# Performance work log

Measured on AMD Instinct MI355X. Metric: run time of the kernel, lower is better.

## Reference

```python
import jax, jax.numpy as jnp
import numpy as np

OBS_DIM, ACTION_DIM, H, FC = 64, 100, 512, 256
IN_DIM = FC + ACTION_DIM


def setup_inputs() -> dict:
    key = jax.random.key(0)
    ks = jax.random.split(key, 10)
    s = lambda k, shp, fan: jax.random.normal(k, shp, jnp.float32) * (1.0 / np.sqrt(fan))
    return {
        "observations": jax.random.normal(ks[0], (32, 2048, OBS_DIM), jnp.float32),
        "actions": jax.random.uniform(ks[1], (32, 2048), jnp.float32),
        "W_obs": s(ks[2], (OBS_DIM, FC), OBS_DIM), "b_obs": jnp.zeros((FC,), jnp.float32),
        "W_act": s(ks[3], (1, ACTION_DIM), 1), "b_act": jnp.zeros((ACTION_DIM,), jnp.float32),
        "W_lstm": s(ks[4], (IN_DIM, 4 * H), IN_DIM),
        "U_lstm": s(ks[5], (H, 4 * H), H),
        "b_lstm": jnp.zeros((4 * H,), jnp.float32),
        "W_proj": s(ks[6], (H, ACTION_DIM), H), "b_proj": jnp.zeros((ACTION_DIM,), jnp.float32),
    }


def _lstm_seq(x, W, U, b):
    # x: [B, T, D] -> outputs [B, T, H]; keras LSTMCell default activations.
    B = x.shape[0]
    h0 = jnp.zeros((B, H), x.dtype)
    c0 = jnp.zeros((B, H), x.dtype)

    def step(carry, x_t):
        h, c = carry
        z = x_t @ W + h @ U + b  # [B, 4H]
        i, f, g, o = jnp.split(z, 4, axis=-1)
        i = jax.nn.sigmoid(i); f = jax.nn.sigmoid(f)
        g = jnp.tanh(g); o = jax.nn.sigmoid(o)
        c = f * c + i * g
        h = o * jnp.tanh(c)
        return (h, c), h

    _, hs = jax.lax.scan(step, (h0, c0), jnp.swapaxes(x, 0, 1))  # [T, B, H]
    return jnp.swapaxes(hs, 0, 1)


def reference(observations, actions, W_obs, b_obs, W_act, b_act,
              W_lstm, U_lstm, b_lstm, W_proj, b_proj):
    a = jax.nn.relu(actions[..., None] @ W_act + b_act)        # [B, T, A]
    ob = jax.nn.relu(observations @ W_obs + b_obs)             # [B, T, FC]
    x = jnp.concatenate([ob, a], axis=-1)                      # [B, T, FC+A]
    seq = _lstm_seq(x, W_lstm, U_lstm, b_lstm)                 # [B, T, H]
    logits = seq @ W_proj + b_proj                             # [B, T, A]
    pi = jax.nn.softmax(logits, axis=-1)
    # tf.math.argmax(logits) defaults to axis=0 (over batch), kept faithfully.
    argmax_actions = jnp.argmax(logits, axis=0)
    return pi, logits, argmax_actions
```

## Files before the change

### kernel.cpp

```cpp
#include <hip/hip_runtime.h>
#include <cstdint>
#include <cstddef>

#define B_   32
#define T_   2048
#define OBS_ 64
#define FC_  256
#define ACT_ 100
#define H_   512
#define TC_  128
#define NCH_ 16

typedef __attribute__((ext_vector_type(4))) unsigned int u32x4;
typedef __attribute__((ext_vector_type(8))) short bf16x8;
typedef __attribute__((ext_vector_type(4))) float f32x4;

static __device__ __forceinline__ bf16x8 as_b(u32x4 v){ union{u32x4 u; bf16x8 b;} x; x.u=v; return x.b; }
static __device__ __forceinline__ unsigned short f2bf(float f){
  unsigned int u = __builtin_bit_cast(unsigned int, f);
  return (unsigned short)((u + 0x7fffu + ((u>>16)&1u)) >> 16);
}
static __device__ __forceinline__ float bf2f(unsigned short s){
  unsigned int u = ((unsigned int)s) << 16;
  return __builtin_bit_cast(float, u);
}
static __device__ __forceinline__ void split3(float v, unsigned short& h, unsigned short& m, unsigned short& l){
  h = f2bf(v);
  float r1 = v - bf2f(h);
  m = f2bf(r1);
  float r2 = r1 - bf2f(m);
  l = f2bf(r2);
}
static __device__ __forceinline__ u32x4 pack8(const unsigned short* v){
  u32x4 r;
  r.x = (unsigned)v[0] | ((unsigned)v[1]<<16);
  r.y = (unsigned)v[2] | ((unsigned)v[3]<<16);
  r.z = (unsigned)v[4] | ((unsigned)v[5]<<16);
  r.w = (unsigned)v[6] | ((unsigned)v[7]<<16);
  return r;
}
static __device__ __forceinline__ u32x4 load_cohx4(const unsigned int* p){
  u32x4 r;
  asm volatile("global_load_dwordx4 %0, %1, off sc0 sc1"
               : "=v"(r) : "v"(p) : "memory");
  return r;
}

static constexpr size_t XF_OFF    = 0;
static constexpr size_t XF_SZ     = (size_t)TC_*2*12*3*64*16;
static constexpr size_t WF_OFF    = XF_OFF + XF_SZ;
static constexpr size_t WF_SZ     = (size_t)32*4*28*3*64*16;
static constexpr size_t WPF_OFF   = WF_OFF + WF_SZ;
static constexpr size_t WPF_SZ    = (size_t)7*16*3*64*16;
static constexpr size_t ZX_OFF    = WPF_OFF + WPF_SZ;
static constexpr size_t ZX_SZ     = (size_t)TC_*2*16*2048*4;
static constexpr size_t HC01_OFF  = ZX_OFF + ZX_SZ;
static constexpr size_t HC01_SZ   = (size_t)TC_*2*16*512*4;
static constexpr size_t HC2_OFF   = HC01_OFF + HC01_SZ;
static constexpr size_t HC2_SZ    = (size_t)TC_*2*16*512*2;
static constexpr size_t HG_OFF    = HC2_OFF + HC2_SZ;
static constexpr size_t HG_SZ     = (size_t)3*2*16*2*256*4;
static constexpr size_t CST_OFF   = HG_OFF + HG_SZ;
static constexpr size_t CST_SZ    = (size_t)B_*H_*8;
static constexpr size_t CTR_OFF   = CST_OFF + CST_SZ;
static constexpr size_t CTR_SZ    = (size_t)2*T_*4;

__global__ __launch_bounds__(256) void k_prep_x(
    const float* __restrict__ obs, const float* __restrict__ act,
    const float* __restrict__ Wobs, const float* __restrict__ bobs,
    const float* __restrict__ Wact, const float* __restrict__ bact,
    u32x4* __restrict__ Xf, int tbase)
{
  __shared__ float Wl[64][257];
  __shared__ float ol[32][64];
  __shared__ float xr[32][256];
  __shared__ float al[32];
  __shared__ float wal[100], bal[100], bol[256];
  int tl = blockIdx.x; int t = tbase + tl; int tid = threadIdx.x;
  for (int i = tid; i < 64*256; i += 256) Wl[i>>8][i&255] = Wobs[i];
  for (int i = tid; i < 32*64; i += 256)
    ol[i>>6][i&63] = obs[((size_t)(i>>6)*T_ + t)*OBS_ + (i&63)];
  if (tid < 32) al[tid] = act[(size_t)tid*T_ + t];
  if (tid < 100) { wal[tid] = Wact[tid]; bal[tid] = bact[tid]; }
  bol[tid] = bobs[tid];
  __syncthreads();
  {
    int k = tid;
    double accd[32];
#pragma unroll
    for (int r = 0; r < 32; ++r) accd[r] = 0.0;
    for (int kc = 0; kc < 64; kc += 8) {
      float w[8];
#pragma unroll
      for (int q = 0; q < 8; ++q) w[q] = Wl[kc+q][k];
#pragma unroll
      for (int r = 0; r < 32; ++r) {
#pragma unroll
        for (int q = 0; q < 8; ++q) accd[r] += (double)w[q]*(double)ol[r][kc+q];
      }
    }
#pragma unroll
    for (int r = 0; r < 32; ++r) xr[r][k] = fmaxf((float)(accd[r] + (double)bol[k]), 0.f);
  }
  __syncthreads();
  int g = tid >> 6, l = tid & 63;
  int r = l & 15, sub = l >> 4;
  for (int p = g; p < 24; p += 4) {
    int bg = p / 12, kk = p % 12;
    int b = bg*16 + r;
    unsigned short vh[8], vm[8], vl[8];
#pragma unroll
    for (int j = 0; j < 8; ++j) {
      int k = kk*32 + sub*8 + j;
      float x;
      if (k < 256)      x = xr[b][k];
      else if (k < 356) {
        double tmp = (double)al[b]*(double)wal[k-256] + (double)bal[k-256];
        x = fmaxf((float)tmp, 0.f);
      } else            x = 0.f;
      split3(x, vh[j], vm[j], vl[j]);
    }
    size_t base = ((((size_t)tl*2 + bg)*12 + kk)*3)*64 + l;
    Xf[base]       = pack8(vh);
    Xf[base + 64]  = pack8(vm);
    Xf[base + 128] = pack8(vl);
  }
}

__global__ __launch_bounds__(256) void k_prep_w(
    const float* __restrict__ Wl, const float* __restrict__ Ul,
    unsigned short* __restrict__ Wf)
{
  size_t gid = (size_t)blockIdx.x*256 + threadIdx.x;
  if (gid >= (size_t)896*2048) return;
  int k = (int)(gid >> 11), oc = (int)(gid & 2047);
  float v = 0.f;
  if (k < 356) v = Wl[(size_t)k*2048 + oc];
  else if (k >= 384) v = Ul[(size_t)(k-384)*2048 + oc];
  unsigned short vh, vm, vlo;
  split3(v, vh, vm, vlo);
  int g = oc >> 9, hs = (oc & 511) >> 4, u = oc & 15;
  int kk = k >> 5, sub = (k >> 3) & 3, j = k & 7;
  size_t e = ((((size_t)(hs*4 + g)*28 + kk)*3 + 0)*64 + (sub*16 + u))*8 + j;
  Wf[e]        = vh;
  Wf[e + 512]  = vm;
  Wf[e + 1024] = vlo;
}

__global__ __launch_bounds__(256) void k_prep_wp(
    const float* __restrict__ Wp, unsigned short* __restrict__ Wpf)
{
  int gid = blockIdx.x*256 + threadIdx.x;
  if (gid >= 512*112) return;
  int k = gid / 112, c = gid % 112;
  float v = (c < 100) ? Wp[(size_t)k*100 + c] : 0.f;
  unsigned short vh, vm, vlo;
  split3(v, vh, vm, vlo);
  int ct = c >> 4, cl = c & 15;
  int kk = k >> 5, sub = (k >> 3) & 3, j = k & 7;
  size_t e = (((size_t)(ct*16 + kk)*3 + 0)*64 + (sub*16 + cl))*8 + j;
  Wpf[e]        = vh;
  Wpf[e + 512]  = vm;
  Wpf[e + 1024] = vlo;
}

__global__ __launch_bounds__(256) void k_prep_zx(
    const u32x4* __restrict__ Xf, const u32x4* __restrict__ Wf,
    float* __restrict__ zx)
{
  int bid = blockIdx.x;
  int hq = bid & 7, bg = (bid >> 3) & 1, tl = bid >> 4;
  int tid = threadIdx.x;
  int g = tid >> 6, lane = tid & 63;
  u32x4 xa[12][3];
  const u32x4* xp = Xf + (((size_t)tl*2 + bg)*12*3)*64 + lane;
#pragma unroll
  for (int f = 0; f < 12; ++f)
#pragma unroll
    for (int p = 0; p < 3; ++p) xa[f][p] = xp[(f*3+p)*64];
  for (int hi = 0; hi < 4; ++hi) {
    int hs = hq*4 + hi;
    const u32x4* bp = Wf + (((size_t)(hs*4 + g)*28)*3)*64 + lane;
    f32x4 a0={0,0,0,0},a1={0,0,0,0},a2={0,0,0,0},a3={0,0,0,0},a4={0,0,0,0},a5={0,0,0,0};
#pragma unroll
    for (int f = 0; f < 12; ++f) {
      u32x4 b0 = bp[(f*3+0)*64], b1 = bp[(f*3+1)*64], b2 = bp[(f*3+2)*64];
      a0 = __builtin_amdgcn_mfma_f32_16x16x32_bf16(as_b(xa[f][0]), as_b(b0), a0, 0,0,0);
      a1 = __builtin_amdgcn_mfma_f32_16x16x32_bf16(as_b(xa[f][0]), as_b(b1), a1, 0,0,0);
      a2 = __builtin_amdgcn_mfma_f32_16x16x32_bf16(as_b(xa[f][1]), as_b(b0), a2, 0,0,0);
      a3 = __builtin_amdgcn_mfma_f32_16x16x32_bf16(as_b(xa[f][0]), as_b(b2), a3, 0,0,0);
      a4 = __builtin_amdgcn_mfma_f32_16x16x32_bf16(as_b(xa[f][2]), as_b(b0), a4, 0,0,0);
      a5 = __builtin_amdgcn_mfma_f32_16x16x32_bf16(as_b(xa[f][1]), as_b(b1), a5, 0,0,0);
    }
    int col = lane & 15;
#pragma unroll
    for (int q = 0; q < 4; ++q) {
      int row = (lane>>4)*4 + q;
      double z = (((double)a3[q]+(double)a4[q])+(double)a5[q])
               + ((double)a1[q]+(double)a2[q]) + (double)a0[q];
      zx[(((size_t)tl*2 + bg)*16 + row)*2048 + g*512 + hs*16 + col] = (float)z;
    }
  }
}

__global__ __launch_bounds__(256, 1) void k_rnn(
    const u32x4* __restrict__ Wf, const float* __restrict__ zx,
    const float* __restrict__ blstm,
    unsigned int* __restrict__ HC01, unsigned short* __restrict__ HC2,
    unsigned int* __restrict__ hg32, int* __restrict__ ctr,
    double* __restrict__ cstate, int tbase)
{
  __shared__ double zbuf[4][16][16];
  __shared__ unsigned int hb01[16][16];
  int wg = blockIdx.x, bg = wg >> 5, hs = wg & 31;
  int tid = threadIdx.x, w = tid >> 6, lane = tid & 63;
  u32x4 Breg[16][3];
  {
    const u32x4* bp = Wf + (((size_t)(hs*4 + w)*28 + 12)*3)*64 + lane;
#pragma unroll
    for (int f = 0; f < 16; ++f)
#pragma unroll
      for (int p = 0; p < 3; ++p) Breg[f][p] = bp[(f*3+p)*64];
  }
  int gr = tid >> 4, gu = tid & 15;
  double bi  = (double)blstm[0*512 + hs*16 + gu];
  double bff = (double)blstm[1*512 + hs*16 + gu];
  double bgg = (double)blstm[2*512 + hs*16 + gu];
  double bo  = (double)blstm[3*512 + hs*16 + gu];
  double c = cstate[(size_t)(bg*16 + gr)*512 + hs*16 + gu];
  int r2 = tid >> 3, p8 = tid & 7;
  int hg0 = hs*16 + 2*p8;
  int pkk = hg0 >> 5, psub = (hg0 >> 3) & 3, pj = hg0 & 7;
  int plw = psub*16 + r2;

#pragma unroll 1
  for (int tl = 0; tl < TC_; ++tl) {
    int gt = tbase + tl;
    int sr = (gt + 2) % 3;
    u32x4 hf[16][2];
    {
      const unsigned int* hbase = hg32 + ((size_t)sr*2 + bg)*16*2*256 + lane*4;
#pragma unroll
      for (int kk = 0; kk < 16; ++kk) {
        hf[kk][0] = load_cohx4(hbase + ((size_t)kk*2 + 0)*256);
        hf[kk][1] = load_cohx4(hbase + ((size_t)kk*2 + 1)*256);
      }
    }
    size_t zrow = (((size_t)tl*2 + bg)*16 + gr)*2048 + hs*16 + gu;
    float z0 = zx[zrow];
    float z1 = zx[zrow + 512];
    float z2 = zx[zrow + 1024];
    float z3 = zx[zrow + 1536];
    asm volatile("s_waitcnt vmcnt(0)" ::: "memory");
    __builtin_amdgcn_sched_barrier(0);
    f32x4 a0={0,0,0,0},a1={0,0,0,0},a2={0,0,0,0},a3={0,0,0,0},a4={0,0,0,0};
#pragma unroll
    for (int kk = 0; kk < 16; ++kk) {
      a0 = __builtin_amdgcn_mfma_f32_16x16x32_bf16(as_b(hf[kk][0]), as_b(Breg[kk][0]), a0, 0,0,0);
      a1 = __builtin_amdgcn_mfma_f32_16x16x32_bf16(as_b(hf[kk][0]), as_b(Breg[kk][1]), a1, 0,0,0);
      a2 = __builtin_amdgcn_mfma_f32_16x16x32_bf16(as_b(hf[kk][1]), as_b(Breg[kk][0]), a2, 0,0,0);
      a3 = __builtin_amdgcn_mfma_f32_16x16x32_bf16(as_b(hf[kk][0]), as_b(Breg[kk][2]), a3, 0,0,0);
      a4 = __builtin_amdgcn_mfma_f32_16x16x32_bf16(as_b(hf[kk][1]), as_b(Breg[kk][1]), a4, 0,0,0);
    }
#pragma unroll
    for (int q = 0; q < 4; ++q)
      zbuf[w][(lane>>4)*4 + q][lane & 15] =
        (((double)a3[q] + (double)a4[q]) + ((double)a1[q] + (double)a2[q])) + (double)a0[q];
    __syncthreads();
    {
      double zi = zbuf[0][gr][gu] + (double)z0 + bi;
      double zf = zbuf[1][gr][gu] + (double)z1 + bff;
      double zg = zbuf[2][gr][gu] + (double)z2 + bgg;
      double zo = zbuf[3][gr][gu] + (double)z3 + bo;
      double i_ = 1.0/(1.0 + exp(-zi));
      double f_ = 1.0/(1.0 + exp(-zf));
      double g_ = tanh(zg);
      double o_ = 1.0/(1.0 + exp(-zo));
      c = f_*c + i_*g_;
      double h = o_*tanh(c);
      unsigned short h0, h1, h2;
      split3((float)h, h0, h1, h2);
      unsigned int w01 = (unsigned)h0 | ((unsigned)h1 << 16);
      size_t hcidx = (((size_t)tl*2 + bg)*16 + gr)*512 + hs*16 + gu;
      HC01[hcidx] = w01;
      HC2[hcidx]  = h2;
      hb01[gr][gu] = w01;
    }
    __syncthreads();
    if (tid < 128) {
      unsigned int a = hb01[r2][2*p8], b = hb01[r2][2*p8+1];
      unsigned int v0 = (a & 0xffffu) | (b << 16);
      unsigned int v1 = (a >> 16)     | (b & 0xffff0000u);
      size_t dg = ((((size_t)(gt%3)*2 + bg)*16 + pkk)*2 + 0)*256 + plw*4 + (pj>>1);
      __hip_atomic_store(&hg32[dg],       v0, __ATOMIC_RELAXED, __HIP_MEMORY_SCOPE_AGENT);
      __hip_atomic_store(&hg32[dg + 256], v1, __ATOMIC_RELAXED, __HIP_MEMORY_SCOPE_AGENT);
    }
    __syncthreads();
    if (tid == 0) {
      __hip_atomic_fetch_add(&ctr[bg*T_ + gt], 1, __ATOMIC_RELAXED, __HIP_MEMORY_SCOPE_AGENT);
      while (__hip_atomic_load(&ctr[bg*T_ + gt], __ATOMIC_RELAXED, __HIP_MEMORY_SCOPE_AGENT) < 32)
        __builtin_amdgcn_s_sleep(1);
    }
    __syncthreads();
  }
  cstate[(size_t)(bg*16 + gr)*512 + hs*16 + gu] = c;
}

__global__ __launch_bounds__(256) void k_logits(
    const unsigned int* __restrict__ HC01, const unsigned short* __restrict__ HC2,
    const u32x4* __restrict__ Wpf,
    const float* __restrict__ bproj, float* __restrict__ out, int tbase)
{
  __shared__ float zl[16][120];
  int bid = blockIdx.x;
  int tl = bid >> 1, bg = bid & 1;
  int tid = threadIdx.x;
  int w = tid >> 6, lane = tid & 63;
  int row = lane & 15, koff = (lane >> 4) * 8;
  u32x4 a[16][3];
  {
    const unsigned int* h01 = HC01 + (((size_t)tl*2 + bg)*16 + row)*512 + koff;
    const unsigned short* h2p = HC2 + (((size_t)tl*2 + bg)*16 + row)*512 + koff;
#pragma unroll
    for (int kk = 0; kk < 16; ++kk) {
      u32x4 c0 = *(const u32x4*)(h01 + 32*kk);
      u32x4 c1 = *(const u32x4*)(h01 + 32*kk + 4);
      u32x4 p0, p1;
      p0.x = (c0.x & 0xffffu) | (c0.y << 16);
      p0.y = (c0.z & 0xffffu) | (c0.w << 16);
      p0.z = (c1.x & 0xffffu) | (c1.y << 16);
      p0.w = (c1.z & 0xffffu) | (c1.w << 16);
      p1.x = (c0.x >> 16) | (c0.y & 0xffff0000u);
      p1.y = (c0.z >> 16) | (c0.w & 0xffff0000u);
      p1.z = (c1.x >> 16) | (c1.y & 0xffff0000u);
      p1.w = (c1.z >> 16) | (c1.w & 0xffff0000u);
      a[kk][0] = p0;
      a[kk][1] = p1;
      a[kk][2] = *(const u32x4*)(h2p + 32*kk);
    }
  }
  for (int ct = w; ct < 7; ct += 4) {
    f32x4 c0 = {0,0,0,0}, c1 = {0,0,0,0}, c2 = {0,0,0,0};
    f32x4 c3 = {0,0,0,0}, c4 = {0,0,0,0}, c5 = {0,0,0,0};
    const u32x4* bp2 = Wpf + ((size_t)ct*16*3)*64 + lane;
#pragma unroll
    for (int kk = 0; kk < 16; ++kk) {
      u32x4 b0 = bp2[(kk*3+0)*64], b1 = bp2[(kk*3+1)*64], b2 = bp2[(kk*3+2)*64];
      c0 = __builtin_amdgcn_mfma_f32_16x16x32_bf16(as_b(a[kk][0]), as_b(b0), c0, 0,0,0);
      c1 = __builtin_amdgcn_mfma_f32_16x16x32_bf16(as_b(a[kk][0]), as_b(b1), c1, 0,0,0);
      c2 = __builtin_amdgcn_mfma_f32_16x16x32_bf16(as_b(a[kk][1]), as_b(b0), c2, 0,0,0);
      c3 = __builtin_amdgcn_mfma_f32_16x16x32_bf16(as_b(a[kk][0]), as_b(b2), c3, 0,0,0);
      c4 = __builtin_amdgcn_mfma_f32_16x16x32_bf16(as_b(a[kk][2]), as_b(b0), c4, 0,0,0);
      c5 = __builtin_amdgcn_mfma_f32_16x16x32_bf16(as_b(a[kk][1]), as_b(b1), c5, 0,0,0);
    }
    int col = ct*16 + (lane & 15);
    float bv = (col < 100) ? bproj[col] : 0.f;
#pragma unroll
    for (int q = 0; q < 4; ++q) {
      double z = (((double)c3[q] + (double)c4[q]) + (double)c5[q])
               + ((double)c1[q] + (double)c2[q]) + (double)c0[q] + (double)bv;
      if (col < 120) zl[(lane>>4)*4 + q][col] = (float)z;
    }
  }
  __syncthreads();
  int srow = tid >> 4, l16 = tid & 15;
  float vv[7];
  float m = -1e30f;
#pragma unroll
  for (int k2 = 0; k2 < 7; ++k2) {
    int col = l16 + 16*k2;
    vv[k2] = (col < 100) ? zl[srow][col] : -1e30f;
    m = fmaxf(m, vv[k2]);
  }
#pragma unroll
  for (int d = 1; d < 16; d <<= 1) m = fmaxf(m, __shfl_xor(m, d, 64));
  float s = 0.f; float ek[7];
#pragma unroll
  for (int k2 = 0; k2 < 7; ++k2) {
    int col = l16 + 16*k2;
    ek[k2] = (col < 100) ? expf(vv[k2] - m) : 0.f;
    s += ek[k2];
  }
#pragma unroll
  for (int d = 1; d < 16; d <<= 1) s += __shfl_xor(s, d, 64);
  int t = tbase + tl; int b = bg*16 + srow;
  float* piout = out;
  float* lgout = out + 6553600ull;
#pragma unroll
  for (int k2 = 0; k2 < 7; ++k2) {
    int col = l16 + 16*k2;
    if (col < 100) {
      size_t idx = ((size_t)b*T_ + t)*100 + col;
      lgout[idx] = vv[k2];
      piout[idx] = ek[k2] / s;
    }
  }
}

__global__ __launch_bounds__(128) void k_argmax(
    const float* __restrict__ lg, float* __restrict__ outA)
{
  int t = blockIdx.x, j = threadIdx.x;
  if (j >= 100) return;
  float best = lg[(size_t)t*100 + j];
  int bi = 0;
  for (int b = 1; b < 32; ++b) {
    float v = lg[((size_t)b*T_ + t)*100 + j];
    if (v > best) { best = v; bi = b; }
  }
  outA[(size_t)t*100 + j] = (float)bi;
}

extern "C" void kernel_launch(void* const* d_in, const int* in_sizes, int n_in,
                              void* d_out, int out_size, void* d_ws, size_t ws_size,
                              hipStream_t stream) {
  const float* obs  = (const float*)d_in[0];
  const float* act  = (const float*)d_in[1];
  const float* Wobs = (const float*)d_in[2];
  const float* bobs = (const float*)d_in[3];
  const float* Wact = (const float*)d_in[4];
  const float* bact = (const float*)d_in[5];
  const float* Wl   = (const float*)d_in[6];
  const float* Ul   = (const float*)d_in[7];
  const float* bl   = (const float*)d_in[8];
  const float* Wp   = (const float*)d_in[9];
  const float* bp   = (const float*)d_in[10];
  char* ws = (char*)d_ws;
  u32x4* Xf             = (u32x4*)(ws + XF_OFF);
  unsigned short* WfS   = (unsigned short*)(ws + WF_OFF);
  unsigned short* WpfS  = (unsigned short*)(ws + WPF_OFF);
  float* zx             = (float*)(ws + ZX_OFF);
  unsigned int* HC01    = (unsigned int*)(ws + HC01_OFF);
  unsigned short* HC2   = (unsigned short*)(ws + HC2_OFF);
  unsigned int* hg32    = (unsigned int*)(ws + HG_OFF);
  double* cstate        = (double*)(ws + CST_OFF);
  int* ctr              = (int*)(ws + CTR_OFF);
  float* out = (float*)d_out;

  hipMemsetAsync(ws + HG_OFF, 0, HG_SZ + CST_SZ + CTR_SZ, stream);
  k_prep_w<<<7168, 256, 0, stream>>>(Wl, Ul, WfS);
  k_prep_wp<<<(512*112 + 255)/256, 256, 0, stream>>>(Wp, WpfS);
  for (int ch = 0; ch < NCH_; ++ch) {
    int tb = ch * TC_;
    k_prep_x<<<TC_, 256, 0, stream>>>(obs, act, Wobs, bobs, Wact, bact, Xf, tb);
    k_prep_zx<<<TC_*2*8, 256, 0, stream>>>((const u32x4*)Xf, (const u32x4*)WfS, zx);
    k_rnn<<<64, 256, 0, stream>>>((const u32x4*)WfS, zx, bl, HC01, HC2,
                                  hg32, ctr, cstate, tb);
    k_logits<<<TC_*2, 256, 0, stream>>>(HC01, HC2, (const u32x4*)WpfS, bp, out, tb);
  }
  k_argmax<<<T_, 128, 0, stream>>>(out + 6553600ull, out + 13107200ull);
}
```

Before: 10.61 ms.

## Interleave LSTM gate columns so each lane computes gates without LDS round-trips

New measurement: 12.99 ms. 22.4% more time.

```diff
diff --git a/kernel.cpp b/kernel.cpp
--- a/kernel.cpp
+++ b/kernel.cpp
@@ -42,7 +42,7 @@
 static __device__ __forceinline__ u32x4 load_cohx4(const unsigned int* p){
   u32x4 r;
   asm volatile("global_load_dwordx4 %0, %1, off sc0 sc1"
-               : "=v"(r) : "v"(p) : "memory");
+               : "=&v"(r) : "v"(p) : "memory");
   return r;
 }
 
@@ -53,7 +53,7 @@
 static constexpr size_t WPF_OFF   = WF_OFF + WF_SZ;
 static constexpr size_t WPF_SZ    = (size_t)7*16*3*64*16;
 static constexpr size_t ZX_OFF    = WPF_OFF + WPF_SZ;
-static constexpr size_t ZX_SZ     = (size_t)TC_*2*16*2048*4;
+static constexpr size_t ZX_SZ     = (size_t)TC_*2*2048*16*4;
 static constexpr size_t HC01_OFF  = ZX_OFF + ZX_SZ;
 static constexpr size_t HC01_SZ   = (size_t)TC_*2*16*512*4;
 static constexpr size_t HC2_OFF   = HC01_OFF + HC01_SZ;
@@ -61,7 +61,7 @@
 static constexpr size_t HG_OFF    = HC2_OFF + HC2_SZ;
 static constexpr size_t HG_SZ     = (size_t)3*2*16*2*256*4;
 static constexpr size_t CST_OFF   = HG_OFF + HG_SZ;
-static constexpr size_t CST_SZ    = (size_t)B_*H_*8;
+static constexpr size_t CST_SZ    = (size_t)B_*H_*4;
 static constexpr size_t CTR_OFF   = CST_OFF + CST_SZ;
 static constexpr size_t CTR_SZ    = (size_t)2*T_*4;
 
@@ -139,9 +139,11 @@
   else if (k >= 384) v = Ul[(size_t)(k-384)*2048 + oc];
   unsigned short vh, vm, vlo;
   split3(v, vh, vm, vlo);
-  int g = oc >> 9, hs = (oc & 511) >> 4, u = oc & 15;
+  int g = oc >> 9, hu = oc & 511;
+  int hs = hu >> 4, wv = (hu >> 2) & 3, u = hu & 3;
+  int cc = g*4 + u;
   int kk = k >> 5, sub = (k >> 3) & 3, j = k & 7;
-  size_t e = ((((size_t)(hs*4 + g)*28 + kk)*3 + 0)*64 + (sub*16 + u))*8 + j;
+  size_t e = ((((size_t)(hs*4 + wv)*28 + kk)*3 + 0)*64 + (sub*16 + cc))*8 + j;
   Wf[e]        = vh;
   Wf[e + 512]  = vm;
   Wf[e + 1024] = vlo;
@@ -166,12 +168,14 @@
 
 __global__ __launch_bounds__(256) void k_prep_zx(
     const u32x4* __restrict__ Xf, const u32x4* __restrict__ Wf,
-    float* __restrict__ zx)
+    const float* __restrict__ blstm, float* __restrict__ zxT)
 {
   int bid = blockIdx.x;
   int hq = bid & 7, bg = (bid >> 3) & 1, tl = bid >> 4;
   int tid = threadIdx.x;
-  int g = tid >> 6, lane = tid & 63;
+  int v = tid >> 6, lane = tid & 63;
+  int cc = lane & 15; int g = cc >> 2, u = cc & 3;
+  int rbase = (lane >> 4) * 4;
   u32x4 xa[12][3];
   const u32x4* xp = Xf + (((size_t)tl*2 + bg)*12*3)*64 + lane;
 #pragma unroll
@@ -180,7 +184,7 @@
     for (int p = 0; p < 3; ++p) xa[f][p] = xp[(f*3+p)*64];
   for (int hi = 0; hi < 4; ++hi) {
     int hs = hq*4 + hi;
-    const u32x4* bp = Wf + (((size_t)(hs*4 + g)*28)*3)*64 + lane;
+    const u32x4* bp = Wf + (((size_t)(hs*4 + v)*28)*3)*64 + lane;
     f32x4 a0={0,0,0,0},a1={0,0,0,0},a2={0,0,0,0},a3={0,0,0,0},a4={0,0,0,0},a5={0,0,0,0};
 #pragma unroll
     for (int f = 0; f < 12; ++f) {
@@ -192,118 +196,132 @@
       a4 = __builtin_amdgcn_mfma_f32_16x16x32_bf16(as_b(xa[f][2]), as_b(b0), a4, 0,0,0);
       a5 = __builtin_amdgcn_mfma_f32_16x16x32_bf16(as_b(xa[f][1]), as_b(b1), a5, 0,0,0);
     }
-    int col = lane & 15;
+    int oc = g*512 + hs*16 + v*4 + u;
+    double bb = (double)blstm[oc];
+    f32x4 st;
 #pragma unroll
     for (int q = 0; q < 4; ++q) {
-      int row = (lane>>4)*4 + q;
       double z = (((double)a3[q]+(double)a4[q])+(double)a5[q])
-               + ((double)a1[q]+(double)a2[q]) + (double)a0[q];
-      zx[(((size_t)tl*2 + bg)*16 + row)*2048 + g*512 + hs*16 + col] = (float)z;
-    }
+               + ((double)a1[q]+(double)a2[q]) + (double)a0[q] + bb;
+      st[q] = (float)z;
+    }
+    *(f32x4*)(zxT + ((size_t)((size_t)(tl*2 + bg)*2048 + oc))*16 + rbase) = st;
   }
 }
 
 __global__ __launch_bounds__(256, 1) void k_rnn(
-    const u32x4* __restrict__ Wf, const float* __restrict__ zx,
-    const float* __restrict__ blstm,
+    const u32x4* __restrict__ Wf, const float* __restrict__ zxT,
     unsigned int* __restrict__ HC01, unsigned short* __restrict__ HC2,
     unsigned int* __restrict__ hg32, int* __restrict__ ctr,
-    double* __restrict__ cstate, int tbase)
-{
-  __shared__ double zbuf[4][16][16];
-  __shared__ unsigned int hb01[16][16];
+    float* __restrict__ cstate, int tbase)
+{
   int wg = blockIdx.x, bg = wg >> 5, hs = wg & 31;
-  int tid = threadIdx.x, w = tid >> 6, lane = tid & 63;
+  int tid = threadIdx.x, wv = tid >> 6, lane = tid & 63;
+  int cc = lane & 15;
+  int g = cc >> 2, u = cc & 3;
+  int rbase = (lane >> 4) * 4;
+  int U = hs*16 + wv*4 + u;
   u32x4 Breg[16][3];
   {
-    const u32x4* bp = Wf + (((size_t)(hs*4 + w)*28 + 12)*3)*64 + lane;
+    const u32x4* bp = Wf + ((((size_t)(hs*4 + wv)*28) + 12)*3)*64 + lane;
 #pragma unroll
     for (int f = 0; f < 16; ++f)
 #pragma unroll
       for (int p = 0; p < 3; ++p) Breg[f][p] = bp[(f*3+p)*64];
-  }
-  int gr = tid >> 4, gu = tid & 15;
-  double bi  = (double)blstm[0*512 + hs*16 + gu];
-  double bff = (double)blstm[1*512 + hs*16 + gu];
-  double bgg = (double)blstm[2*512 + hs*16 + gu];
-  double bo  = (double)blstm[3*512 + hs*16 + gu];
-  double c = cstate[(size_t)(bg*16 + gr)*512 + hs*16 + gu];
-  int r2 = tid >> 3, p8 = tid & 7;
-  int hg0 = hs*16 + 2*p8;
-  int pkk = hg0 >> 5, psub = (hg0 >> 3) & 3, pj = hg0 & 7;
-  int plw = psub*16 + r2;
+#pragma unroll
+    for (int f = 0; f < 16; ++f)
+#pragma unroll
+      for (int p = 0; p < 3; ++p) asm volatile("" : "+v"(Breg[f][p]));
+  }
+  float c[4];
+#pragma unroll
+  for (int q = 0; q < 4; ++q)
+    c[q] = cstate[(size_t)(bg*16 + rbase + q)*512 + U];
+  int Ue = hs*16 + wv*4 + (u & 2);
+  int wkk = Ue >> 5, wsub = (Ue >> 3) & 3, wwrd = (Ue >> 1) & 3;
 
 #pragma unroll 1
   for (int tl = 0; tl < TC_; ++tl) {
     int gt = tbase + tl;
-    int sr = (gt + 2) % 3;
-    u32x4 hf[16][2];
+    u32x4 hf0[16], hf1[16];
     {
-      const unsigned int* hbase = hg32 + ((size_t)sr*2 + bg)*16*2*256 + lane*4;
+      const unsigned int* hbase = hg32 + ((size_t)((gt+2)%3)*2 + bg)*16*2*256 + lane*4;
 #pragma unroll
       for (int kk = 0; kk < 16; ++kk) {
-        hf[kk][0] = load_cohx4(hbase + ((size_t)kk*2 + 0)*256);
-        hf[kk][1] = load_cohx4(hbase + ((size_t)kk*2 + 1)*256);
+        hf0[kk] = load_cohx4(hbase + (kk*2+0)*256);
+        hf1[kk] = load_cohx4(hbase + (kk*2+1)*256);
       }
     }
-    size_t zrow = (((size_t)tl*2 + bg)*16 + gr)*2048 + hs*16 + gu;
-    float z0 = zx[zrow];
-    float z1 = zx[zrow + 512];
-    float z2 = zx[zrow + 1024];
-    float z3 = zx[zrow + 1536];
+    f32x4 zx = *(const f32x4*)(zxT + ((size_t)((size_t)(tl*2 + bg)*2048 + g*512 + U))*16 + rbase);
     asm volatile("s_waitcnt vmcnt(0)" ::: "memory");
     __builtin_amdgcn_sched_barrier(0);
     f32x4 a0={0,0,0,0},a1={0,0,0,0},a2={0,0,0,0},a3={0,0,0,0},a4={0,0,0,0};
 #pragma unroll
     for (int kk = 0; kk < 16; ++kk) {
-      a0 = __builtin_amdgcn_mfma_f32_16x16x32_bf16(as_b(hf[kk][0]), as_b(Breg[kk][0]), a0, 0,0,0);
-      a1 = __builtin_amdgcn_mfma_f32_16x16x32_bf16(as_b(hf[kk][0]), as_b(Breg[kk][1]), a1, 0,0,0);
-      a2 = __builtin_amdgcn_mfma_f32_16x16x32_bf16(as_b(hf[kk][1]), as_b(Breg[kk][0]), a2, 0,0,0);
-      a3 = __builtin_amdgcn_mfma_f32_16x16x32_bf16(as_b(hf[kk][0]), as_b(Breg[kk][2]), a3, 0,0,0);
-      a4 = __builtin_amdgcn_mfma_f32_16x16x32_bf16(as_b(hf[kk][1]), as_b(Breg[kk][1]), a4, 0,0,0);
-    }
-#pragma unroll
-    for (int q = 0; q < 4; ++q)
-      zbuf[w][(lane>>4)*4 + q][lane & 15] =
-        (((double)a3[q] + (double)a4[q]) + ((double)a1[q] + (double)a2[q])) + (double)a0[q];
-    __syncthreads();
-    {
-      double zi = zbuf[0][gr][gu] + (double)z0 + bi;
-      double zf = zbuf[1][gr][gu] + (double)z1 + bff;
-      double zg = zbuf[2][gr][gu] + (double)z2 + bgg;
-      double zo = zbuf[3][gr][gu] + (double)z3 + bo;
-      double i_ = 1.0/(1.0 + exp(-zi));
-      double f_ = 1.0/(1.0 + exp(-zf));
-      double g_ = tanh(zg);
-      double o_ = 1.0/(1.0 + exp(-zo));
-      c = f_*c + i_*g_;
-      double h = o_*tanh(c);
-      unsigned short h0, h1, h2;
-      split3((float)h, h0, h1, h2);
-      unsigned int w01 = (unsigned)h0 | ((unsigned)h1 << 16);
-      size_t hcidx = (((size_t)tl*2 + bg)*16 + gr)*512 + hs*16 + gu;
-      HC01[hcidx] = w01;
-      HC2[hcidx]  = h2;
-      hb01[gr][gu] = w01;
-    }
-    __syncthreads();
-    if (tid < 128) {
-      unsigned int a = hb01[r2][2*p8], b = hb01[r2][2*p8+1];
-      unsigned int v0 = (a & 0xffffu) | (b << 16);
-      unsigned int v1 = (a >> 16)     | (b & 0xffff0000u);
-      size_t dg = ((((size_t)(gt%3)*2 + bg)*16 + pkk)*2 + 0)*256 + plw*4 + (pj>>1);
-      __hip_atomic_store(&hg32[dg],       v0, __ATOMIC_RELAXED, __HIP_MEMORY_SCOPE_AGENT);
-      __hip_atomic_store(&hg32[dg + 256], v1, __ATOMIC_RELAXED, __HIP_MEMORY_SCOPE_AGENT);
-    }
-    __syncthreads();
-    if (tid == 0) {
-      __hip_atomic_fetch_add(&ctr[bg*T_ + gt], 1, __ATOMIC_RELAXED, __HIP_MEMORY_SCOPE_AGENT);
-      while (__hip_atomic_load(&ctr[bg*T_ + gt], __ATOMIC_RELAXED, __HIP_MEMORY_SCOPE_AGENT) < 32)
-        __builtin_amdgcn_s_sleep(1);
-    }
-    __syncthreads();
-  }
-  cstate[(size_t)(bg*16 + gr)*512 + hs*16 + gu] = c;
+      a0 = __builtin_amdgcn_mfma_f32_16x16x32_bf16(as_b(hf0[kk]), as_b(Breg[kk][0]), a0, 0,0,0);
+      a1 = __builtin_amdgcn_mfma_f32_16x16x32_bf16(as_b(hf0[kk]), as_b(Breg[kk][1]), a1, 0,0,0);
+      a2 = __builtin_amdgcn_mfma_f32_16x16x32_bf16(as_b(hf1[kk]), as_b(Breg[kk][0]), a2, 0,0,0);
+      a3 = __builtin_amdgcn_mfma_f32_16x16x32_bf16(as_b(hf0[kk]), as_b(Breg[kk][2]), a3, 0,0,0);
+      a4 = __builtin_amdgcn_mfma_f32_16x16x32_bf16(as_b(hf1[kk]), as_b(Breg[kk][1]), a4, 0,0,0);
+    }
+    float hv[4];
+#pragma unroll
+    for (int q = 0; q < 4; ++q) {
+      float z = (float)(((double)a3[q] + (double)a4[q])
+                      + ((double)a1[q] + (double)a2[q]) + (double)a0[q]) + zx[q];
+      float o0 = __shfl_xor(z, 4, 64);
+      float e0 = (g & 1) ? o0 : z;
+      float e1 = (g & 1) ? z  : o0;
+      float p0 = __shfl_xor(e0, 8, 64);
+      float p1 = __shfl_xor(e1, 8, 64);
+      float zi = (g & 2) ? p0 : e0;
+      float zf = (g & 2) ? p1 : e1;
+      float zg = (g & 2) ? e0 : p0;
+      float zo = (g & 2) ? e1 : p1;
+      float i_ = 1.f/(1.f + expf(-zi));
+      float f_ = 1.f/(1.f + expf(-zf));
+      float g_ = tanhf(zg);
+      float o_ = 1.f/(1.f + expf(-zo));
+      c[q] = f_*c[q] + i_*g_;
+      hv[q] = o_*tanhf(c[q]);
+    }
+    unsigned int* ringW = hg32 + ((size_t)(gt%3)*2 + bg)*16*2*256;
+#pragma unroll
+    for (int q = 0; q < 4; ++q) {
+      float hq = hv[q];
+      float hp = __shfl_xor(hq, 1, 64);
+      unsigned short h0o = f2bf(hq);
+      float r1 = hq - bf2f(h0o);
+      unsigned short h1o = f2bf(r1);
+      if (g == 0) {
+        unsigned short h2o = f2bf(r1 - bf2f(h1o));
+        size_t hcidx = ((size_t)(tl*2 + bg)*16 + rbase + q)*512 + U;
+        HC01[hcidx] = (unsigned)h0o | ((unsigned)h1o << 16);
+        HC2[hcidx]  = h2o;
+        if (!(u & 1)) {
+          unsigned short h0p = f2bf(hp);
+          unsigned short h1p = f2bf(hp - bf2f(h0p));
+          unsigned int w0 = (unsigned)h0o | ((unsigned)h0p << 16);
+          unsigned int w1 = (unsigned)h1o | ((unsigned)h1p << 16);
+          size_t d0 = ((size_t)wkk*2 + 0)*256 + (wsub*16 + rbase + q)*4 + wwrd;
+          __hip_atomic_store(&ringW[d0],       w0, __ATOMIC_RELAXED, __HIP_MEMORY_SCOPE_AGENT);
+          __hip_atomic_store(&ringW[d0 + 256], w1, __ATOMIC_RELAXED, __HIP_MEMORY_SCOPE_AGENT);
+        }
+      }
+    }
+    if (tl < TC_-1) {
+      __syncthreads();
+      if (tid == 0) {
+        __hip_atomic_fetch_add(&ctr[bg*T_ + gt], 1, __ATOMIC_RELAXED, __HIP_MEMORY_SCOPE_AGENT);
+        while (__hip_atomic_load(&ctr[bg*T_ + gt], __ATOMIC_RELAXED, __HIP_MEMORY_SCOPE_AGENT) < 32)
+          __builtin_amdgcn_s_sleep(1);
+      }
+      __syncthreads();
+    }
+  }
+#pragma unroll
+  for (int q = 0; q < 4; ++q)
+    if (g == 0) cstate[(size_t)(bg*16 + rbase + q)*512 + U] = c[q];
 }
 
 __global__ __launch_bounds__(256) void k_logits(
@@ -429,11 +447,11 @@
   u32x4* Xf             = (u32x4*)(ws + XF_OFF);
   unsigned short* WfS   = (unsigned short*)(ws + WF_OFF);
   unsigned short* WpfS  = (unsigned short*)(ws + WPF_OFF);
-  float* zx             = (float*)(ws + ZX_OFF);
+  float* zxT            = (float*)(ws + ZX_OFF);
   unsigned int* HC01    = (unsigned int*)(ws + HC01_OFF);
   unsigned short* HC2   = (unsigned short*)(ws + HC2_OFF);
   unsigned int* hg32    = (unsigned int*)(ws + HG_OFF);
-  double* cstate        = (double*)(ws + CST_OFF);
+  float* cstate         = (float*)(ws + CST_OFF);
   int* ctr              = (int*)(ws + CTR_OFF);
   float* out = (float*)d_out;
 
@@ -443,8 +461,8 @@
   for (int ch = 0; ch < NCH_; ++ch) {
     int tb = ch * TC_;
     k_prep_x<<<TC_, 256, 0, stream>>>(obs, act, Wobs, bobs, Wact, bact, Xf, tb);
-    k_prep_zx<<<TC_*2*8, 256, 0, stream>>>((const u32x4*)Xf, (const u32x4*)WfS, zx);
-    k_rnn<<<64, 256, 0, stream>>>((const u32x4*)WfS, zx, bl, HC01, HC2,
+    k_prep_zx<<<TC_*2*8, 256, 0, stream>>>((const u32x4*)Xf, (const u32x4*)WfS, bl, zxT);
+    k_rnn<<<64, 256, 0, stream>>>((const u32x4*)WfS, zxT, HC01, HC2,
                                   hg32, ctr, cstate, tb);
     k_logits<<<TC_*2, 256, 0, stream>>>(HC01, HC2, (const u32x4*)WpfS, bp, out, tb);
   }
```
